# Performance work log

Measured on AMD Instinct MI355X. Metric: run time of the kernel, lower is better.

Reference implementation:

```python
import jax, jax.numpy as jnp
import numpy as np

EPS = 1e-5

@jax.custom_vjp
def binarize(x):
    # sign quantization: {-1, +1} (0 -> +1), as in BinaryNet Binarize
    return jnp.where(x >= 0, 1.0, -1.0).astype(x.dtype)

def _bin_fwd(x):
    return binarize(x), x

def _bin_bwd(res, g):
    # straight-through estimator with hardtanh clipping
    return (g * (jnp.abs(res) <= 1.0).astype(g.dtype),)

binarize.defvjp(_bin_fwd, _bin_bwd)


def batchnorm(x, gamma, beta):
    # BatchNorm1d, training mode: biased batch statistics over the batch axis
    mu = jnp.mean(x, axis=0)
    var = jnp.var(x, axis=0)
    return (x - mu) * jax.lax.rsqrt(var + EPS) * gamma + beta


def setup_inputs() -> dict:
    key = jax.random.key(0)
    ks = jax.random.split(key, 5)
    B, IND, HID, OUT = 16384, 768, 4096, 10
    return {
        "x": jax.random.normal(ks[0], (B, 784), jnp.float32),
        "w1": jax.random.normal(ks[1], (HID, IND), jnp.float32) * 0.05,
        "w2": jax.random.normal(ks[2], (HID, HID), jnp.float32) * 0.05,
        "w3": jax.random.normal(ks[3], (HID, HID), jnp.float32) * 0.05,
        "w4": jax.random.normal(ks[4], (OUT, HID), jnp.float32) * 0.05,
        "g1": jnp.ones(HID, jnp.float32), "b1": jnp.zeros(HID, jnp.float32),
        "g2": jnp.ones(HID, jnp.float32), "b2": jnp.zeros(HID, jnp.float32),
        "g3": jnp.ones(HID, jnp.float32), "b3": jnp.zeros(HID, jnp.float32),
        "g4": jnp.ones(OUT, jnp.float32), "b4": jnp.zeros(OUT, jnp.float32),
    }


def reference(x, w1, w2, w3, w4, g1, b1, g2, b2, g3, b3, g4, b4):
    # x.view(-1, 784); if width == 784, keep first 768 features
    h = x.reshape(-1, 784)[:, :768]
    # BinarizeLinear: binarize activations (width != 784) and weights, then matmul
    h = binarize(h) @ binarize(w1).T            # [B, 4096]
    h = jnp.clip(batchnorm(h, g1, b1), -1.0, 1.0)  # bn1 + hardtanh1
    h = binarize(h) @ binarize(w2).T
    h = jnp.clip(batchnorm(h, g2, b2), -1.0, 1.0)
    h = binarize(h) @ binarize(w3).T
    h = jnp.clip(batchnorm(h, g3, b3), -1.0, 1.0)
    h = binarize(h) @ binarize(w4).T            # [B, 10]
    h = batchnorm(h, g4, b4)
    return jax.nn.log_softmax(h, axis=1)
```

## Files before the change

### kernel.cpp

```cpp
#include <hip/hip_runtime.h>
#include <hip/hip_bf16.h>
#include <stdint.h>

typedef int v4i __attribute__((ext_vector_type(4)));

#define DEVI static __device__ __forceinline__

DEVI void gload16(const void* g, void* l) {
    __builtin_amdgcn_global_load_lds(
        (const __attribute__((address_space(1))) void*)g,
        (__attribute__((address_space(3))) void*)l,
        16, 0, 0);
}

#define WAITV(n) asm volatile("s_waitcnt vmcnt(" #n ")" ::: "memory")
#define WAITL0() asm volatile("s_waitcnt lgkmcnt(0)" ::: "memory")
#define SBAR()   __builtin_amdgcn_s_barrier()
#define SCHEDB() __builtin_amdgcn_sched_barrier(0)

__global__ __launch_bounds__(256) void k_bin_f32_to_i8(
    const float* __restrict__ w, int8_t* __restrict__ o, int n16)
{
    int t = blockIdx.x * 256 + threadIdx.x;
    if (t >= n16) return;
    const float4* s = (const float4*)w + (size_t)t * 4;
    union { int4 v; int8_t b[16]; } u;
#pragma unroll
    for (int i = 0; i < 4; ++i) {
        float4 f = s[i];
        u.b[i*4+0] = (f.x >= 0.f) ? (int8_t)1 : (int8_t)-1;
        u.b[i*4+1] = (f.y >= 0.f) ? (int8_t)1 : (int8_t)-1;
        u.b[i*4+2] = (f.z >= 0.f) ? (int8_t)1 : (int8_t)-1;
        u.b[i*4+3] = (f.w >= 0.f) ? (int8_t)1 : (int8_t)-1;
    }
    *(int4*)(o + (size_t)t * 16) = u.v;
}

__global__ __launch_bounds__(256) void k_bin_x(
    const float* __restrict__ x, int8_t* __restrict__ o)
{
    int t = blockIdx.x * 256 + threadIdx.x;
    int row = t / 48;
    int ch  = t % 48;
    const float4* s = (const float4*)(x + (size_t)row * 784 + ch * 16);
    union { int4 v; int8_t b[16]; } u;
#pragma unroll
    for (int i = 0; i < 4; ++i) {
        float4 f = s[i];
        u.b[i*4+0] = (f.x >= 0.f) ? (int8_t)1 : (int8_t)-1;
        u.b[i*4+1] = (f.y >= 0.f) ? (int8_t)1 : (int8_t)-1;
        u.b[i*4+2] = (f.z >= 0.f) ? (int8_t)1 : (int8_t)-1;
        u.b[i*4+3] = (f.w >= 0.f) ? (int8_t)1 : (int8_t)-1;
    }
    *(int4*)(o + (size_t)row * 768 + ch * 16) = u.v;
}

__global__ __launch_bounds__(512, 2)
void k_gemm256(const int8_t* __restrict__ A, const int8_t* __restrict__ B,
               int16_t* __restrict__ C, int* __restrict__ gsum,
               unsigned long long* __restrict__ gsq,
               int N, int K, int nbx)
{
    __shared__ __align__(16) int8_t lds[131072];

    const int tid  = threadIdx.x;
    const int lane = tid & 63;
    const int wave = tid >> 6;

    const int cpx = gridDim.x >> 3;
    const int id  = blockIdx.x;
    const int sw  = (id & 7) * cpx + (id >> 3);
    const int bx  = sw % nbx;
    const int by  = sw / nbx;

    const int NT = K >> 6;

    const int sr  = tid >> 2;
    const int asw = (((tid & 3) ^ (sr & 3)) << 4);
    const int8_t* gA0 = A + (size_t)(by * 256 + sr)       * K + asw;
    const int8_t* gA1 = A + (size_t)(by * 256 + 128 + sr) * K + asw;
    const int8_t* gB0 = B + (size_t)(bx * 256 + sr)       * K + asw;
    const int8_t* gB1 = B + (size_t)(bx * 256 + 128 + sr) * K + asw;
    const int ld0 = (wave * 64) << 4;
    const int ld1 = (512 + wave * 64) << 4;

    const int lrow = lane & 15;
    const int ksl  = lane >> 4;
    const int wr = (wave >> 2) * 128;
    const int wc = (wave & 3) * 64;
    const int fsw = ((ksl ^ (lrow & 3)) << 4);
    int aoff[8], boff[4];
#pragma unroll
    for (int m = 0; m < 8; ++m) aoff[m] = ((wr + m * 16 + lrow) << 6) + fsw;
#pragma unroll
    for (int n = 0; n < 4; ++n) boff[n] = ((wc + n * 16 + lrow) << 6) + fsw;

    v4i acc[8][4];
    v4i zero = {0, 0, 0, 0};
#pragma unroll
    for (int m = 0; m < 8; ++m)
#pragma unroll
        for (int n = 0; n < 4; ++n) acc[m][n] = zero;

#define STAGE_A(kt, b) do { const int _o = (kt) << 6;                    \
        int8_t* _d = lds + (b) * 16384;                                  \
        gload16(gA0 + _o, _d + ld0); gload16(gA1 + _o, _d + ld1); } while (0)
#define STAGE_B(kt, b) do { const int _o = (kt) << 6;                    \
        int8_t* _d = lds + 65536 + (b) * 16384;                          \
        gload16(gB0 + _o, _d + ld0); gload16(gB1 + _o, _d + ld1); } while (0)

    STAGE_A(0, 0); STAGE_B(0, 0);
    STAGE_A(1, 1); STAGE_B(1, 1);
    STAGE_A(2, 2); STAGE_B(2, 2);
    WAITV(8);
    SBAR();

    for (int kt = 0; kt < NT; ++kt) {
        const int b = kt & 3;
        const int8_t* ab = lds + b * 16384;
        const int8_t* bb = lds + 65536 + b * 16384;
        const int sb = (kt + 3) & 3;
        const bool st = (kt + 3 < NT);

        v4i af[4], bf[4];
#pragma unroll
        for (int m = 0; m < 4; ++m) af[m] = *(const v4i*)(ab + aoff[m]);
#pragma unroll
        for (int n = 0; n < 4; ++n) bf[n] = *(const v4i*)(bb + boff[n]);
        if (st) STAGE_A(kt + 3, sb);
        SBAR();
        WAITL0();
        SCHEDB();
        __builtin_amdgcn_s_setprio(1);
#pragma unroll
        for (int m = 0; m < 4; ++m)
#pragma unroll
            for (int n = 0; n < 4; ++n)
                acc[m][n] = __builtin_amdgcn_mfma_i32_16x16x64_i8(
                    af[m], bf[n], acc[m][n], 0, 0, 0);
        __builtin_amdgcn_s_setprio(0);
        SBAR();

        v4i ag[4];
#pragma unroll
        for (int m = 0; m < 4; ++m) ag[m] = *(const v4i*)(ab + aoff[4 + m]);
        if (st) STAGE_B(kt + 3, sb);
        if (kt < NT - 3)       { WAITV(8); }
        else if (kt == NT - 3) { WAITV(4); }
        else if (kt == NT - 2) { WAITV(0); }
        SBAR();
        WAITL0();
        SCHEDB();
        __builtin_amdgcn_s_setprio(1);
#pragma unroll
        for (int m = 0; m < 4; ++m)
#pragma unroll
            for (int n = 0; n < 4; ++n)
                acc[4 + m][n] = __builtin_amdgcn_mfma_i32_16x16x64_i8(
                    ag[m], bf[n], acc[4 + m][n], 0, 0, 0);
        __builtin_amdgcn_s_setprio(0);
        SBAR();
    }
#undef STAGE_A
#undef STAGE_B

    const int row0 = by * 256 + wr + ksl * 4;
    const int col0 = bx * 256 + wc + lrow;
#pragma unroll
    for (int m = 0; m < 8; ++m)
#pragma unroll
        for (int rr = 0; rr < 4; ++rr) {
            int16_t* dst = C + (size_t)(row0 + m * 16 + rr) * N + col0;
#pragma unroll
            for (int n = 0; n < 4; ++n)
                dst[n * 16] = (int16_t)acc[m][n][rr];
        }
#pragma unroll
    for (int n = 0; n < 4; ++n) {
        int s = 0; unsigned q = 0;
#pragma unroll
        for (int m = 0; m < 8; ++m)
#pragma unroll
            for (int rr = 0; rr < 4; ++rr) {
                int v = acc[m][n][rr];
                s += v;
                q += (unsigned)(v * v);
            }
        s += __shfl_xor(s, 16);
        s += __shfl_xor(s, 32);
        q += (unsigned)__shfl_xor((int)q, 16);
        q += (unsigned)__shfl_xor((int)q, 32);
        if (ksl == 0) {
            const int col = col0 + n * 16;
            atomicAdd(&gsum[col], s);
            atomicAdd(&gsq[col], (unsigned long long)q);
        }
    }
}

__global__ __launch_bounds__(256)
void k_gemm4(const int8_t* __restrict__ A, const int8_t* __restrict__ Bw,
             int* __restrict__ C4, int K)
{
    const int lane = threadIdx.x & 63;
    const int wave = threadIdx.x >> 6;
    const int lrow = lane & 15, ksl = lane >> 4;
    const int r0 = blockIdx.x * 128 + wave * 32;
    const int k0 = blockIdx.y * 512;

    const int8_t* ap0 = A + (size_t)(r0 + lrow) * K + k0 + ksl * 16;
    const int8_t* ap1 = ap0 + (size_t)16 * K;
    const int8_t* bp  = Bw + (size_t)lrow * K + k0 + ksl * 16;

    v4i acc0 = {0,0,0,0}, acc1 = {0,0,0,0};
#pragma unroll
    for (int kk = 0; kk < 8; ++kk) {
        v4i a0 = *(const v4i*)(ap0 + kk * 64);
        v4i a1 = *(const v4i*)(ap1 + kk * 64);
        v4i b  = *(const v4i*)(bp  + kk * 64);
        acc0 = __builtin_amdgcn_mfma_i32_16x16x64_i8(a0, b, acc0, 0, 0, 0);
        acc1 = __builtin_amdgcn_mfma_i32_16x16x64_i8(a1, b, acc1, 0, 0, 0);
    }
#pragma unroll
    for (int rr = 0; rr < 4; ++rr) {
        atomicAdd(&C4[(size_t)(r0 + ksl * 4 + rr) * 16 + lrow], acc0[rr]);
        atomicAdd(&C4[(size_t)(r0 + 16 + ksl * 4 + rr) * 16 + lrow], acc1[rr]);
    }
}

__global__ __launch_bounds__(256)
void k_colstats4(const int* __restrict__ C4, int rows,
                 int* __restrict__ gsum, unsigned long long* __restrict__ gsq)
{
    const int col = threadIdx.x & 15, grp = threadIdx.x >> 4;
    const int rpb = rows / gridDim.x;
    const int r0  = blockIdx.x * rpb;
    int s = 0; unsigned long long q = 0;
    for (int r = grp; r < rpb; r += 16) {
        int v = C4[(size_t)(r0 + r) * 16 + col];
        s += v;
        q += (unsigned long long)((long long)v * (long long)v);
    }
    __shared__ int ss[256];
    __shared__ unsigned long long sq[256];
    ss[threadIdx.x] = s; sq[threadIdx.x] = q;
    __syncthreads();
    if (grp == 0) {
#pragma unroll
        for (int t = 1; t < 16; ++t) { s += ss[t * 16 + col]; q += sq[t * 16 + col]; }
        atomicAdd(&gsum[col], s);
        atomicAdd(&gsq[col], q);
    }
}

__global__ __launch_bounds__(128)
void k_finalize(const int* __restrict__ gsum, const unsigned long long* __restrict__ gsq,
                const float* __restrict__ gamma, const float* __restrict__ beta,
                float* __restrict__ pa, float* __restrict__ pb,
                int rows, int ncols_act, int ncols_pad)
{
    int c = blockIdx.x * 128 + threadIdx.x;
    if (c >= ncols_pad) return;
    double mu  = (double)gsum[c] / (double)rows;
    double var = (double)(long long)gsq[c] / (double)rows - mu * mu;
    float rs = rsqrtf((float)var + 1e-5f);
    float g  = (c < ncols_act) ? gamma[c] : 0.f;
    float be = (c < ncols_act) ? beta[c]  : 0.f;
    pa[c] = rs * g;
    pb[c] = be - (float)mu * rs * g;
}

__global__ __launch_bounds__(256)
void k_bnbin(const int16_t* __restrict__ C, const float* __restrict__ pa,
             const float* __restrict__ pb, int8_t* __restrict__ Aout,
             int n16, int colmask)
{
    int t = blockIdx.x * 256 + threadIdx.x;
    if (t >= n16) return;
    const size_t base = (size_t)t * 16;
    const int c0 = (int)(base & (size_t)colmask);
    union { int4 v; short s[8]; } u0, u1;
    u0.v = *(const int4*)(C + base);
    u1.v = *(const int4*)(C + base + 8);
    float4 a[4], b[4];
#pragma unroll
    for (int i = 0; i < 4; ++i) {
        a[i] = *(const float4*)(pa + c0 + i * 4);
        b[i] = *(const float4*)(pb + c0 + i * 4);
    }
    union { int4 v; int8_t b[16]; } o;
#pragma unroll
    for (int i = 0; i < 16; ++i) {
        float y = (float)((i < 8) ? u0.s[i] : u1.s[i - 8]);
        float aa = ((const float*)&a[i >> 2])[i & 3];
        float bb = ((const float*)&b[i >> 2])[i & 3];
        o.b[i] = (y * aa + bb >= 0.f) ? (int8_t)1 : (int8_t)-1;
    }
    *(int4*)(Aout + base) = o.v;
}

__global__ __launch_bounds__(256)
void k_logsoftmax(const int* __restrict__ C4, const float* __restrict__ pa,
                  const float* __restrict__ pb, float* __restrict__ out, int rows)
{
    int r = blockIdx.x * 256 + threadIdx.x;
    if (r >= rows) return;
    const int* row = C4 + (size_t)r * 16;
    float v[10];
    float m = -1e30f;
#pragma unroll
    for (int c = 0; c < 10; ++c) {
        v[c] = (float)row[c] * pa[c] + pb[c];
        m = fmaxf(m, v[c]);
    }
    float s = 0.f;
#pragma unroll
    for (int c = 0; c < 10; ++c) s += expf(v[c] - m);
    float ls = logf(s);
#pragma unroll
    for (int c = 0; c < 10; ++c) out[(size_t)r * 10 + c] = v[c] - m - ls;
}

extern "C" void kernel_launch(void* const* d_in, const int* in_sizes, int n_in,
                              void* d_out, int out_size, void* d_ws, size_t ws_size,
                              hipStream_t stream)
{
    (void)in_sizes; (void)n_in; (void)out_size; (void)ws_size;
    const float* x  = (const float*)d_in[0];
    const float* w1 = (const float*)d_in[1];
    const float* w2 = (const float*)d_in[2];
    const float* w3 = (const float*)d_in[3];
    const float* w4 = (const float*)d_in[4];
    const float* g1 = (const float*)d_in[5];
    const float* b1 = (const float*)d_in[6];
    const float* g2 = (const float*)d_in[7];
    const float* b2 = (const float*)d_in[8];
    const float* g3 = (const float*)d_in[9];
    const float* b3 = (const float*)d_in[10];
    const float* g4 = (const float*)d_in[11];
    const float* b4 = (const float*)d_in[12];
    float* out = (float*)d_out;

    const int B = 16384, HID = 4096, IND = 768;

    char* p = (char*)d_ws;
    size_t off = 0;
    auto alloc = [&](size_t sz) -> char* {
        char* r = p + off;
        off += (sz + 255) & ~(size_t)255;
        return r;
    };
    int8_t*  W1   = (int8_t*)alloc((size_t)HID * IND);
    int8_t*  W2   = (int8_t*)alloc((size_t)HID * HID);
    int8_t*  W3   = (int8_t*)alloc((size_t)HID * HID);
    int8_t*  W4p  = (int8_t*)alloc((size_t)16 * HID);
    int8_t*  Abuf = (int8_t*)alloc((size_t)B * HID);
    int16_t* C    = (int16_t*)alloc((size_t)B * HID * 2);
    int*     C4   = (int*)alloc((size_t)B * 16 * 4);
    int*     gsum = (int*)alloc((size_t)HID * 4);
    unsigned long long* gsq = (unsigned long long*)alloc((size_t)HID * 8);
    float*   pa   = (float*)alloc((size_t)HID * 4);
    float*   pb   = (float*)alloc((size_t)HID * 4);

    hipMemsetAsync(W4p, 0, (size_t)16 * HID, stream);
    k_bin_f32_to_i8<<<(HID * IND / 16 + 255) / 256, 256, 0, stream>>>(w1, W1, HID * IND / 16);
    k_bin_f32_to_i8<<<(HID * HID / 16 + 255) / 256, 256, 0, stream>>>(w2, W2, HID * HID / 16);
    k_bin_f32_to_i8<<<(HID * HID / 16 + 255) / 256, 256, 0, stream>>>(w3, W3, HID * HID / 16);
    k_bin_f32_to_i8<<<(10 * HID / 16 + 255) / 256, 256, 0, stream>>>(w4, W4p, 10 * HID / 16);
    k_bin_x<<<B * 48 / 256, 256, 0, stream>>>(x, Abuf);

    const int nbx = HID / 256, nby = B / 256;

    hipMemsetAsync(gsum, 0, HID * 12, stream);
    k_gemm256<<<nbx * nby, 512, 0, stream>>>(Abuf, W1, C, gsum, gsq, HID, IND, nbx);
    k_finalize<<<HID / 128, 128, 0, stream>>>(gsum, gsq, g1, b1, pa, pb, B, HID, HID);
    k_bnbin<<<B * HID / 16 / 256, 256, 0, stream>>>(C, pa, pb, Abuf, B * HID / 16, HID - 1);

    hipMemsetAsync(gsum, 0, HID * 12, stream);
    k_gemm256<<<nbx * nby, 512, 0, stream>>>(Abuf, W2, C, gsum, gsq, HID, HID, nbx);
    k_finalize<<<HID / 128, 128, 0, stream>>>(gsum, gsq, g2, b2, pa, pb, B, HID, HID);
    k_bnbin<<<B * HID / 16 / 256, 256, 0, stream>>>(C, pa, pb, Abuf, B * HID / 16, HID - 1);

    hipMemsetAsync(gsum, 0, HID * 12, stream);
    k_gemm256<<<nbx * nby, 512, 0, stream>>>(Abuf, W3, C, gsum, gsq, HID, HID, nbx);
    k_finalize<<<HID / 128, 128, 0, stream>>>(gsum, gsq, g3, b3, pa, pb, B, HID, HID);
    k_bnbin<<<B * HID / 16 / 256, 256, 0, stream>>>(C, pa, pb, Abuf, B * HID / 16, HID - 1);

    hipMemsetAsync(C4, 0, (size_t)B * 16 * 4, stream);
    k_gemm4<<<dim3(B / 128, 8), 256, 0, stream>>>(Abuf, W4p, C4, HID);
    hipMemsetAsync(gsum, 0, HID * 12, stream);
    k_colstats4<<<16, 256, 0, stream>>>(C4, B, gsum, gsq);
    k_finalize<<<1, 128, 0, stream>>>(gsum, gsq, g4, b4, pa, pb, B, 10, 16);
    k_logsoftmax<<<B / 256, 256, 0, stream>>>(C4, pa, pb, out, B);
}
```

Measured before the change: 835.3 us.

## Prefetch next-tile LDS fragments into registers and cut barriers per K step

Result: faster. 799.5 us (-4.3%).

```diff
diff --git a/kernel.cpp b/kernel.cpp
--- a/kernel.cpp
+++ b/kernel.cpp
@@ -14,9 +14,7 @@
 }
 
 #define WAITV(n) asm volatile("s_waitcnt vmcnt(" #n ")" ::: "memory")
-#define WAITL0() asm volatile("s_waitcnt lgkmcnt(0)" ::: "memory")
 #define SBAR()   __builtin_amdgcn_s_barrier()
-#define SCHEDB() __builtin_amdgcn_sched_barrier(0)
 
 __global__ __launch_bounds__(256) void k_bin_f32_to_i8(
     const float* __restrict__ w, int8_t* __restrict__ o, int n16)
@@ -76,7 +74,7 @@
     const int NT = K >> 6;
 
     const int sr  = tid >> 2;
-    const int asw = (((tid & 3) ^ (sr & 3)) << 4);
+    const int asw = (((tid & 3) ^ ((sr >> 1) & 3)) << 4);
     const int8_t* gA0 = A + (size_t)(by * 256 + sr)       * K + asw;
     const int8_t* gA1 = A + (size_t)(by * 256 + 128 + sr) * K + asw;
     const int8_t* gB0 = B + (size_t)(bx * 256 + sr)       * K + asw;
@@ -88,7 +86,7 @@
     const int ksl  = lane >> 4;
     const int wr = (wave >> 2) * 128;
     const int wc = (wave & 3) * 64;
-    const int fsw = ((ksl ^ (lrow & 3)) << 4);
+    const int fsw = ((ksl ^ ((lrow >> 1) & 3)) << 4);
     int aoff[8], boff[4];
 #pragma unroll
     for (int m = 0; m < 8; ++m) aoff[m] = ((wr + m * 16 + lrow) << 6) + fsw;
@@ -112,54 +110,84 @@
     STAGE_A(0, 0); STAGE_B(0, 0);
     STAGE_A(1, 1); STAGE_B(1, 1);
     STAGE_A(2, 2); STAGE_B(2, 2);
-    WAITV(8);
+    WAITV(4);
     SBAR();
 
-    for (int kt = 0; kt < NT; ++kt) {
-        const int b = kt & 3;
-        const int8_t* ab = lds + b * 16384;
-        const int8_t* bb = lds + 65536 + b * 16384;
-        const int sb = (kt + 3) & 3;
-        const bool st = (kt + 3 < NT);
-
-        v4i af[4], bf[4];
-#pragma unroll
-        for (int m = 0; m < 4; ++m) af[m] = *(const v4i*)(ab + aoff[m]);
-#pragma unroll
-        for (int n = 0; n < 4; ++n) bf[n] = *(const v4i*)(bb + boff[n]);
-        if (st) STAGE_A(kt + 3, sb);
-        SBAR();
-        WAITL0();
-        SCHEDB();
+    v4i afC[4], bfC[4];
+    {
+        const int8_t* ab = lds;
+        const int8_t* bb = lds + 65536;
+#pragma unroll
+        for (int m = 0; m < 4; ++m) afC[m] = *(const v4i*)(ab + aoff[m]);
+#pragma unroll
+        for (int n = 0; n < 4; ++n) bfC[n] = *(const v4i*)(bb + boff[n]);
+    }
+
+    for (int kt = 0; kt < NT - 1; ++kt) {
+        const int b  = kt & 3;
+        const int nb = (kt + 1) & 3;
+        const int8_t* ab  = lds + b * 16384;
+        const int8_t* abN = lds + nb * 16384;
+        const int8_t* bbN = lds + 65536 + nb * 16384;
+
+        if (kt + 3 < NT) { const int sb = (kt + 3) & 3; STAGE_A(kt + 3, sb); STAGE_B(kt + 3, sb); }
+        if (kt < NT - 3)       { WAITV(4); }
+        else if (kt == NT - 3) { WAITV(0); }
+
+        v4i ag[4];
+#pragma unroll
+        for (int m = 0; m < 4; ++m) ag[m] = *(const v4i*)(ab + aoff[4 + m]);
+
         __builtin_amdgcn_s_setprio(1);
 #pragma unroll
         for (int m = 0; m < 4; ++m)
 #pragma unroll
             for (int n = 0; n < 4; ++n)
                 acc[m][n] = __builtin_amdgcn_mfma_i32_16x16x64_i8(
-                    af[m], bf[n], acc[m][n], 0, 0, 0);
+                    afC[m], bfC[n], acc[m][n], 0, 0, 0);
         __builtin_amdgcn_s_setprio(0);
-        SBAR();
-
-        v4i ag[4];
-#pragma unroll
-        for (int m = 0; m < 4; ++m) ag[m] = *(const v4i*)(ab + aoff[4 + m]);
-        if (st) STAGE_B(kt + 3, sb);
-        if (kt < NT - 3)       { WAITV(8); }
-        else if (kt == NT - 3) { WAITV(4); }
-        else if (kt == NT - 2) { WAITV(0); }
-        SBAR();
-        WAITL0();
-        SCHEDB();
+
+        v4i afN[4], bfN[4];
+#pragma unroll
+        for (int m = 0; m < 4; ++m) afN[m] = *(const v4i*)(abN + aoff[m]);
+#pragma unroll
+        for (int n = 0; n < 4; ++n) bfN[n] = *(const v4i*)(bbN + boff[n]);
+
         __builtin_amdgcn_s_setprio(1);
 #pragma unroll
         for (int m = 0; m < 4; ++m)
 #pragma unroll
             for (int n = 0; n < 4; ++n)
                 acc[4 + m][n] = __builtin_amdgcn_mfma_i32_16x16x64_i8(
-                    ag[m], bf[n], acc[4 + m][n], 0, 0, 0);
+                    ag[m], bfC[n], acc[4 + m][n], 0, 0, 0);
         __builtin_amdgcn_s_setprio(0);
+
         SBAR();
+#pragma unroll
+        for (int m = 0; m < 4; ++m) afC[m] = afN[m];
+#pragma unroll
+        for (int n = 0; n < 4; ++n) bfC[n] = bfN[n];
+    }
+
+    {
+        const int8_t* ab = lds + ((NT - 1) & 3) * 16384;
+        v4i ag[4];
+#pragma unroll
+        for (int m = 0; m < 4; ++m) ag[m] = *(const v4i*)(ab + aoff[4 + m]);
+        __builtin_amdgcn_s_setprio(1);
+#pragma unroll
+        for (int m = 0; m < 4; ++m)
+#pragma unroll
+            for (int n = 0; n < 4; ++n)
+                acc[m][n] = __builtin_amdgcn_mfma_i32_16x16x64_i8(
+                    afC[m], bfC[n], acc[m][n], 0, 0, 0);
+#pragma unroll
+        for (int m = 0; m < 4; ++m)
+#pragma unroll
+            for (int n = 0; n < 4; ++n)
+                acc[4 + m][n] = __builtin_amdgcn_mfma_i32_16x16x64_i8(
+                    ag[m], bfC[n], acc[4 + m][n], 0, 0, 0);
+        __builtin_amdgcn_s_setprio(0);
     }
 #undef STAGE_A
 #undef STAGE_B
```

## Shrink int8 GEMM tile to 128x128 with register double-buffered fragments

Applied to the files above, without the earlier changes.

Measured after the change: 975.1 us. +16.7%, slower.

```diff
diff --git a/kernel.cpp b/kernel.cpp
--- a/kernel.cpp
+++ b/kernel.cpp
@@ -14,9 +14,7 @@
 }
 
 #define WAITV(n) asm volatile("s_waitcnt vmcnt(" #n ")" ::: "memory")
-#define WAITL0() asm volatile("s_waitcnt lgkmcnt(0)" ::: "memory")
 #define SBAR()   __builtin_amdgcn_s_barrier()
-#define SCHEDB() __builtin_amdgcn_sched_barrier(0)
 
 __global__ __launch_bounds__(256) void k_bin_f32_to_i8(
     const float* __restrict__ w, int8_t* __restrict__ o, int n16)
@@ -55,13 +53,13 @@
     *(int4*)(o + (size_t)row * 768 + ch * 16) = u.v;
 }
 
-__global__ __launch_bounds__(512, 2)
-void k_gemm256(const int8_t* __restrict__ A, const int8_t* __restrict__ B,
-               int16_t* __restrict__ C, int* __restrict__ gsum,
-               unsigned long long* __restrict__ gsq,
-               int N, int K, int nbx)
-{
-    __shared__ __align__(16) int8_t lds[131072];
+__global__ __launch_bounds__(256, 2)
+void k_gemm(const int8_t* __restrict__ A, const int8_t* __restrict__ B,
+            int16_t* __restrict__ C, int* __restrict__ gsum,
+            unsigned long long* __restrict__ gsq,
+            int N, int K, int nbx)
+{
+    __shared__ __align__(16) int8_t lds[65536];
 
     const int tid  = threadIdx.x;
     const int lane = tid & 63;
@@ -76,98 +74,81 @@
     const int NT = K >> 6;
 
     const int sr  = tid >> 2;
-    const int asw = (((tid & 3) ^ (sr & 3)) << 4);
-    const int8_t* gA0 = A + (size_t)(by * 256 + sr)       * K + asw;
-    const int8_t* gA1 = A + (size_t)(by * 256 + 128 + sr) * K + asw;
-    const int8_t* gB0 = B + (size_t)(bx * 256 + sr)       * K + asw;
-    const int8_t* gB1 = B + (size_t)(bx * 256 + 128 + sr) * K + asw;
-    const int ld0 = (wave * 64) << 4;
-    const int ld1 = (512 + wave * 64) << 4;
+    const int asw = (((tid & 3) ^ ((sr >> 1) & 3)) << 4);
+    const int8_t* gA0 = A + (size_t)(by * 128 + sr)      * K + asw;
+    const int8_t* gA1 = A + (size_t)(by * 128 + 64 + sr) * K + asw;
+    const int8_t* gB0 = B + (size_t)(bx * 128 + sr)      * K + asw;
+    const int8_t* gB1 = B + (size_t)(bx * 128 + 64 + sr) * K + asw;
+    const int ldw = wave << 10;
 
     const int lrow = lane & 15;
     const int ksl  = lane >> 4;
-    const int wr = (wave >> 2) * 128;
-    const int wc = (wave & 3) * 64;
-    const int fsw = ((ksl ^ (lrow & 3)) << 4);
-    int aoff[8], boff[4];
-#pragma unroll
-    for (int m = 0; m < 8; ++m) aoff[m] = ((wr + m * 16 + lrow) << 6) + fsw;
+    const int wr = (wave >> 1) * 64;
+    const int wc = (wave & 1) * 64;
+    const int fsw = ((ksl ^ ((lrow >> 1) & 3)) << 4);
+    int aoff[4], boff[4];
+#pragma unroll
+    for (int m = 0; m < 4; ++m) aoff[m] = ((wr + m * 16 + lrow) << 6) + fsw;
 #pragma unroll
     for (int n = 0; n < 4; ++n) boff[n] = ((wc + n * 16 + lrow) << 6) + fsw;
 
-    v4i acc[8][4];
+    v4i acc[4][4];
     v4i zero = {0, 0, 0, 0};
 #pragma unroll
-    for (int m = 0; m < 8; ++m)
+    for (int m = 0; m < 4; ++m)
 #pragma unroll
         for (int n = 0; n < 4; ++n) acc[m][n] = zero;
 
-#define STAGE_A(kt, b) do { const int _o = (kt) << 6;                    \
-        int8_t* _d = lds + (b) * 16384;                                  \
-        gload16(gA0 + _o, _d + ld0); gload16(gA1 + _o, _d + ld1); } while (0)
-#define STAGE_B(kt, b) do { const int _o = (kt) << 6;                    \
-        int8_t* _d = lds + 65536 + (b) * 16384;                          \
-        gload16(gB0 + _o, _d + ld0); gload16(gB1 + _o, _d + ld1); } while (0)
-
-    STAGE_A(0, 0); STAGE_B(0, 0);
-    STAGE_A(1, 1); STAGE_B(1, 1);
-    STAGE_A(2, 2); STAGE_B(2, 2);
-    WAITV(8);
+#define STAGE(kt) do { const int _o = (kt) << 6; const int _b = ((kt) & 3) << 13; \
+        gload16(gA0 + _o, lds + _b + ldw);                                        \
+        gload16(gA1 + _o, lds + _b + 4096 + ldw);                                 \
+        gload16(gB0 + _o, lds + 32768 + _b + ldw);                                \
+        gload16(gB1 + _o, lds + 32768 + _b + 4096 + ldw); } while (0)
+
+#define READF(da, db, slot) do {                                                  \
+        const int8_t* _ab = lds + ((slot) << 13);                                 \
+        const int8_t* _bb = lds + 32768 + ((slot) << 13);                         \
+        _Pragma("unroll") for (int m = 0; m < 4; ++m)                             \
+            da[m] = *(const v4i*)(_ab + aoff[m]);                                 \
+        _Pragma("unroll") for (int n = 0; n < 4; ++n)                             \
+            db[n] = *(const v4i*)(_bb + boff[n]); } while (0)
+
+#define MFMA16(fa, fb) do {                                                       \
+        __builtin_amdgcn_s_setprio(1);                                            \
+        _Pragma("unroll") for (int m = 0; m < 4; ++m)                             \
+        _Pragma("unroll") for (int n = 0; n < 4; ++n)                             \
+            acc[m][n] = __builtin_amdgcn_mfma_i32_16x16x64_i8(                    \
+                fa[m], fb[n], acc[m][n], 0, 0, 0);                                \
+        __builtin_amdgcn_s_setprio(0); } while (0)
+
+#define TILE(kt, ca, cb, na, nb) do {                                             \
+        if ((kt) + 3 < NT) STAGE((kt) + 3);                                       \
+        if ((kt) < NT - 3)       { WAITV(4); }                                    \
+        else if ((kt) == NT - 3) { WAITV(0); }                                    \
+        if ((kt) + 1 < NT) READF(na, nb, ((kt) + 1) & 3);                         \
+        MFMA16(ca, cb);                                                           \
+        SBAR(); } while (0)
+
+    STAGE(0); STAGE(1); STAGE(2);
+    WAITV(4);
     SBAR();
 
-    for (int kt = 0; kt < NT; ++kt) {
-        const int b = kt & 3;
-        const int8_t* ab = lds + b * 16384;
-        const int8_t* bb = lds + 65536 + b * 16384;
-        const int sb = (kt + 3) & 3;
-        const bool st = (kt + 3 < NT);
-
-        v4i af[4], bf[4];
-#pragma unroll
-        for (int m = 0; m < 4; ++m) af[m] = *(const v4i*)(ab + aoff[m]);
-#pragma unroll
-        for (int n = 0; n < 4; ++n) bf[n] = *(const v4i*)(bb + boff[n]);
-        if (st) STAGE_A(kt + 3, sb);
-        SBAR();
-        WAITL0();
-        SCHEDB();
-        __builtin_amdgcn_s_setprio(1);
-#pragma unroll
-        for (int m = 0; m < 4; ++m)
-#pragma unroll
-            for (int n = 0; n < 4; ++n)
-                acc[m][n] = __builtin_amdgcn_mfma_i32_16x16x64_i8(
-                    af[m], bf[n], acc[m][n], 0, 0, 0);
-        __builtin_amdgcn_s_setprio(0);
-        SBAR();
-
-        v4i ag[4];
-#pragma unroll
-        for (int m = 0; m < 4; ++m) ag[m] = *(const v4i*)(ab + aoff[4 + m]);
-        if (st) STAGE_B(kt + 3, sb);
-        if (kt < NT - 3)       { WAITV(8); }
-        else if (kt == NT - 3) { WAITV(4); }
-        else if (kt == NT - 2) { WAITV(0); }
-        SBAR();
-        WAITL0();
-        SCHEDB();
-        __builtin_amdgcn_s_setprio(1);
-#pragma unroll
-        for (int m = 0; m < 4; ++m)
-#pragma unroll
-            for (int n = 0; n < 4; ++n)
-                acc[4 + m][n] = __builtin_amdgcn_mfma_i32_16x16x64_i8(
-                    ag[m], bf[n], acc[4 + m][n], 0, 0, 0);
-        __builtin_amdgcn_s_setprio(0);
-        SBAR();
-    }
-#undef STAGE_A
-#undef STAGE_B
-
-    const int row0 = by * 256 + wr + ksl * 4;
-    const int col0 = bx * 256 + wc + lrow;
-#pragma unroll
-    for (int m = 0; m < 8; ++m)
+    v4i aX[4], bX[4], aY[4], bY[4];
+    READF(aX, bX, 0);
+
+    for (int kt2 = 0; kt2 < NT; kt2 += 2) {
+        TILE(kt2,     aX, bX, aY, bY);
+        TILE(kt2 + 1, aY, bY, aX, bX);
+    }
+#undef STAGE
+#undef READF
+#undef MFMA16
+#undef TILE
+
+    const int row0 = by * 128 + wr + ksl * 4;
+    const int col0 = bx * 128 + wc + lrow;
+#pragma unroll
+    for (int m = 0; m < 4; ++m)
 #pragma unroll
         for (int rr = 0; rr < 4; ++rr) {
             int16_t* dst = C + (size_t)(row0 + m * 16 + rr) * N + col0;
@@ -179,7 +160,7 @@
     for (int n = 0; n < 4; ++n) {
         int s = 0; unsigned q = 0;
 #pragma unroll
-        for (int m = 0; m < 8; ++m)
+        for (int m = 0; m < 4; ++m)
 #pragma unroll
             for (int rr = 0; rr < 4; ++rr) {
                 int v = acc[m][n][rr];
@@ -369,20 +350,20 @@
     k_bin_f32_to_i8<<<(10 * HID / 16 + 255) / 256, 256, 0, stream>>>(w4, W4p, 10 * HID / 16);
     k_bin_x<<<B * 48 / 256, 256, 0, stream>>>(x, Abuf);
 
-    const int nbx = HID / 256, nby = B / 256;
+    const int nbx = HID / 128, nby = B / 128;
 
     hipMemsetAsync(gsum, 0, HID * 12, stream);
-    k_gemm256<<<nbx * nby, 512, 0, stream>>>(Abuf, W1, C, gsum, gsq, HID, IND, nbx);
+    k_gemm<<<nbx * nby, 256, 0, stream>>>(Abuf, W1, C, gsum, gsq, HID, IND, nbx);
     k_finalize<<<HID / 128, 128, 0, stream>>>(gsum, gsq, g1, b1, pa, pb, B, HID, HID);
     k_bnbin<<<B * HID / 16 / 256, 256, 0, stream>>>(C, pa, pb, Abuf, B * HID / 16, HID - 1);
 
     hipMemsetAsync(gsum, 0, HID * 12, stream);
-    k_gemm256<<<nbx * nby, 512, 0, stream>>>(Abuf, W2, C, gsum, gsq, HID, HID, nbx);
+    k_gemm<<<nbx * nby, 256, 0, stream>>>(Abuf, W2, C, gsum, gsq, HID, HID, nbx);
     k_finalize<<<HID / 128, 128, 0, stream>>>(gsum, gsq, g2, b2, pa, pb, B, HID, HID);
     k_bnbin<<<B * HID / 16 / 256, 256, 0, stream>>>(C, pa, pb, Abuf, B * HID / 16, HID - 1);
 
     hipMemsetAsync(gsum, 0, HID * 12, stream);
-    k_gemm256<<<nbx * nby, 512, 0, stream>>>(Abuf, W3, C, gsum, gsq, HID, HID, nbx);
+    k_gemm<<<nbx * nby, 256, 0, stream>>>(Abuf, W3, C, gsum, gsq, HID, HID, nbx);
     k_finalize<<<HID / 128, 128, 0, stream>>>(gsum, gsq, g3, b3, pa, pb, B, HID, HID);
     k_bnbin<<<B * HID / 16 / 256, 256, 0, stream>>>(C, pa, pb, Abuf, B * HID / 16, HID - 1);
 
```

## Double-buffer LDS fragment registers and prefetch next tile during MFMA

Applied to the files above, without the earlier changes.

Measured after the change: 803.8 us. 1.04x faster.

```diff
diff --git a/kernel.cpp b/kernel.cpp
--- a/kernel.cpp
+++ b/kernel.cpp
@@ -14,9 +14,7 @@
 }
 
 #define WAITV(n) asm volatile("s_waitcnt vmcnt(" #n ")" ::: "memory")
-#define WAITL0() asm volatile("s_waitcnt lgkmcnt(0)" ::: "memory")
 #define SBAR()   __builtin_amdgcn_s_barrier()
-#define SCHEDB() __builtin_amdgcn_sched_barrier(0)
 
 __global__ __launch_bounds__(256) void k_bin_f32_to_i8(
     const float* __restrict__ w, int8_t* __restrict__ o, int n16)
@@ -76,7 +74,7 @@
     const int NT = K >> 6;
 
     const int sr  = tid >> 2;
-    const int asw = (((tid & 3) ^ (sr & 3)) << 4);
+    const int asw = (((tid & 3) ^ ((sr >> 1) & 3)) << 4);
     const int8_t* gA0 = A + (size_t)(by * 256 + sr)       * K + asw;
     const int8_t* gA1 = A + (size_t)(by * 256 + 128 + sr) * K + asw;
     const int8_t* gB0 = B + (size_t)(bx * 256 + sr)       * K + asw;
@@ -88,7 +86,7 @@
     const int ksl  = lane >> 4;
     const int wr = (wave >> 2) * 128;
     const int wc = (wave & 3) * 64;
-    const int fsw = ((ksl ^ (lrow & 3)) << 4);
+    const int fsw = ((ksl ^ ((lrow >> 1) & 3)) << 4);
     int aoff[8], boff[4];
 #pragma unroll
     for (int m = 0; m < 8; ++m) aoff[m] = ((wr + m * 16 + lrow) << 6) + fsw;
@@ -102,67 +100,84 @@
 #pragma unroll
         for (int n = 0; n < 4; ++n) acc[m][n] = zero;
 
-#define STAGE_A(kt, b) do { const int _o = (kt) << 6;                    \
-        int8_t* _d = lds + (b) * 16384;                                  \
-        gload16(gA0 + _o, _d + ld0); gload16(gA1 + _o, _d + ld1); } while (0)
-#define STAGE_B(kt, b) do { const int _o = (kt) << 6;                    \
-        int8_t* _d = lds + 65536 + (b) * 16384;                          \
-        gload16(gB0 + _o, _d + ld0); gload16(gB1 + _o, _d + ld1); } while (0)
-
-    STAGE_A(0, 0); STAGE_B(0, 0);
-    STAGE_A(1, 1); STAGE_B(1, 1);
-    STAGE_A(2, 2); STAGE_B(2, 2);
-    WAITV(8);
+#define STAGE_A(kt) do { const int _o = (kt) << 6; const int _b = ((kt) & 3) * 16384; \
+        gload16(gA0 + _o, lds + _b + ld0); gload16(gA1 + _o, lds + _b + ld1); } while (0)
+#define STAGE_B(kt) do { const int _o = (kt) << 6; const int _b = ((kt) & 3) * 16384; \
+        gload16(gB0 + _o, lds + 65536 + _b + ld0); gload16(gB1 + _o, lds + 65536 + _b + ld1); } while (0)
+
+#define READF(da, db, slot) do {                                                  \
+        const int8_t* _ab = lds + ((slot) * 16384);                               \
+        const int8_t* _bb = lds + 65536 + ((slot) * 16384);                       \
+        _Pragma("unroll") for (int m = 0; m < 4; ++m)                             \
+            da[m] = *(const v4i*)(_ab + aoff[m]);                                 \
+        _Pragma("unroll") for (int n = 0; n < 4; ++n)                             \
+            db[n] = *(const v4i*)(_bb + boff[n]); } while (0)
+
+#define TILEF(kt, CA, CB, NA, NB) do {                                            \
+        const int8_t* _ab = lds + (((kt) & 3) * 16384);                           \
+        if ((kt) + 3 < NT) STAGE_A((kt) + 3);                                     \
+        v4i _ag[4];                                                               \
+        _Pragma("unroll") for (int m = 0; m < 4; ++m)                             \
+            _ag[m] = *(const v4i*)(_ab + aoff[4 + m]);                            \
+        SBAR();                                                                   \
+        __builtin_amdgcn_s_setprio(1);                                            \
+        _Pragma("unroll") for (int m = 0; m < 4; ++m)                             \
+        _Pragma("unroll") for (int n = 0; n < 4; ++n)                             \
+            acc[m][n] = __builtin_amdgcn_mfma_i32_16x16x64_i8(                    \
+                CA[m], CB[n], acc[m][n], 0, 0, 0);                                \
+        __builtin_amdgcn_s_setprio(0);                                            \
+        SBAR();                                                                   \
+        if ((kt) + 3 < NT) STAGE_B((kt) + 3);                                     \
+        if ((kt) < NT - 3)       { WAITV(4); }                                    \
+        else if ((kt) == NT - 3) { WAITV(0); }                                    \
+        READF(NA, NB, ((kt) + 1) & 3);                                            \
+        SBAR();                                                                   \
+        __builtin_amdgcn_s_setprio(1);                                            \
+        _Pragma("unroll") for (int m = 0; m < 4; ++m)                             \
+        _Pragma("unroll") for (int n = 0; n < 4; ++n)                             \
+            acc[4 + m][n] = __builtin_amdgcn_mfma_i32_16x16x64_i8(                \
+                _ag[m], CB[n], acc[4 + m][n], 0, 0, 0);                           \
+        __builtin_amdgcn_s_setprio(0);                                            \
+        SBAR(); } while (0)
+
+    STAGE_A(0); STAGE_B(0);
+    STAGE_A(1); STAGE_B(1);
+    STAGE_A(2); STAGE_B(2);
+    WAITV(4);
     SBAR();
 
-    for (int kt = 0; kt < NT; ++kt) {
-        const int b = kt & 3;
-        const int8_t* ab = lds + b * 16384;
-        const int8_t* bb = lds + 65536 + b * 16384;
-        const int sb = (kt + 3) & 3;
-        const bool st = (kt + 3 < NT);
-
-        v4i af[4], bf[4];
-#pragma unroll
-        for (int m = 0; m < 4; ++m) af[m] = *(const v4i*)(ab + aoff[m]);
-#pragma unroll
-        for (int n = 0; n < 4; ++n) bf[n] = *(const v4i*)(bb + boff[n]);
-        if (st) STAGE_A(kt + 3, sb);
-        SBAR();
-        WAITL0();
-        SCHEDB();
+    v4i aX[4], bX[4], aY[4], bY[4];
+    READF(aX, bX, 0);
+
+    for (int kt = 0; kt < NT - 2; kt += 2) {
+        TILEF(kt,     aX, bX, aY, bY);
+        TILEF(kt + 1, aY, bY, aX, bX);
+    }
+    TILEF(NT - 2, aX, bX, aY, bY);
+    {
+        const int8_t* _ab = lds + (((NT - 1) & 3) * 16384);
+        v4i ag[4];
+#pragma unroll
+        for (int m = 0; m < 4; ++m) ag[m] = *(const v4i*)(_ab + aoff[4 + m]);
         __builtin_amdgcn_s_setprio(1);
 #pragma unroll
         for (int m = 0; m < 4; ++m)
 #pragma unroll
             for (int n = 0; n < 4; ++n)
                 acc[m][n] = __builtin_amdgcn_mfma_i32_16x16x64_i8(
-                    af[m], bf[n], acc[m][n], 0, 0, 0);
-        __builtin_amdgcn_s_setprio(0);
-        SBAR();
-
-        v4i ag[4];
-#pragma unroll
-        for (int m = 0; m < 4; ++m) ag[m] = *(const v4i*)(ab + aoff[4 + m]);
-        if (st) STAGE_B(kt + 3, sb);
-        if (kt < NT - 3)       { WAITV(8); }
-        else if (kt == NT - 3) { WAITV(4); }
-        else if (kt == NT - 2) { WAITV(0); }
-        SBAR();
-        WAITL0();
-        SCHEDB();
-        __builtin_amdgcn_s_setprio(1);
+                    aY[m], bY[n], acc[m][n], 0, 0, 0);
 #pragma unroll
         for (int m = 0; m < 4; ++m)
 #pragma unroll
             for (int n = 0; n < 4; ++n)
                 acc[4 + m][n] = __builtin_amdgcn_mfma_i32_16x16x64_i8(
-                    ag[m], bf[n], acc[4 + m][n], 0, 0, 0);
+                    ag[m], bY[n], acc[4 + m][n], 0, 0, 0);
         __builtin_amdgcn_s_setprio(0);
-        SBAR();
     }
 #undef STAGE_A
 #undef STAGE_B
+#undef READF
+#undef TILEF
 
     const int row0 = by * 256 + wr + ksl * 4;
     const int col0 = bx * 256 + wc + lrow;
```
